# Kernel optimization log

Hardware: AMD Instinct MI355X
Metric: run time of the kernel (lower is better)

Reference implementation:

```python
import jax, jax.numpy as jnp
import numpy as np

TEMPERATURE = 0.5
SCALE_LOSS = 1.0 / 32.0
LAMBDA = 0.0039


def setup_inputs() -> dict:
    key = jax.random.key(0)
    z = jax.random.normal(key, (4096, 6, 256), dtype=jnp.float32)
    return {"z": z}


def reference(z):
    B, V = z.shape[0], z.shape[1]
    # [B, V, ...] -> [V, B, D], L2-normalize embeddings
    zv = z.reshape(B, V, -1).transpose(1, 0, 2)
    zn = zv / jnp.linalg.norm(zv, axis=-1, keepdims=True)

    # Positive error: per-sample cross-view similarity [B, V, V]
    sim_pos = jnp.einsum('vbd,wbd->bvw', zn, zn)
    pos = jnp.exp((1.0 - sim_pos) / TEMPERATURE).mean(axis=(1, 2))  # [B]

    # Negative error: per-view within-batch similarity [V, B, B]
    sim_neg = jnp.exp(jnp.einsum('vbd,vcd->vbc', zn, zn) / TEMPERATURE)
    offdiag_mask = ~jnp.eye(B, dtype=bool)  # [B, B]
    off_mean = jnp.where(offdiag_mask[None], sim_neg, 0.0).sum(-1) / (B - 1)  # [V, B]
    neg = off_mean.sum(0)  # [B], accumulated over views

    return jnp.sum(pos) * SCALE_LOSS + LAMBDA * jnp.sum(neg)
```

## Files before the change

### kernel.cpp

```cpp
#include <hip/hip_runtime.h>
#include <cstdint>
#include <cstddef>

#define B_N 4096
#define V_N 6
#define D_N 256
#define NTILE 528

typedef __bf16 bf16x8 __attribute__((ext_vector_type(8)));
typedef float f32x4 __attribute__((ext_vector_type(4)));

#define ALPHA 1.41421356237309515f

__device__ __forceinline__ unsigned short f2bf(float f) {
  unsigned int u = __float_as_uint(f);
  unsigned int r = (u + 0x7fffu + ((u >> 16) & 1u)) >> 16;
  return (unsigned short)r;
}

__device__ __forceinline__ void async_load16(void* lds, const void* gmem) {
  __builtin_amdgcn_global_load_lds(
      (const __attribute__((address_space(1))) unsigned int*)gmem,
      (__attribute__((address_space(3))) unsigned int*)lds,
      16, 0, 0);
}

__global__ __launch_bounds__(256) void norm_pos_kernel(
    const float* __restrict__ z, unsigned short* __restrict__ znb,
    float* __restrict__ pos_part) {
  const int b = blockIdx.x;
  const int t = threadIdx.x;
  const int lane = t & 63;
  const int w = t >> 6;

  __shared__ float zs[V_N][D_N];
  __shared__ float red[V_N][4];
  __shared__ float inv[V_N];
  __shared__ float pred[4];

  const float* zb = z + (size_t)b * (V_N * D_N);
#pragma unroll
  for (int v = 0; v < V_N; ++v) zs[v][t] = zb[v * D_N + t];
  __syncthreads();

#pragma unroll
  for (int v = 0; v < V_N; ++v) {
    float x = zs[v][t];
    float s = x * x;
#pragma unroll
    for (int off = 32; off > 0; off >>= 1) s += __shfl_down(s, off);
    if (lane == 0) red[v][w] = s;
  }
  __syncthreads();
  if (t < V_N) inv[t] = rsqrtf(red[t][0] + red[t][1] + red[t][2] + red[t][3]);
  __syncthreads();

#pragma unroll
  for (int v = 0; v < V_N; ++v) {
    float zn = zs[v][t] * inv[v] * ALPHA;
    znb[((size_t)v * B_N + b) * D_N + t] = f2bf(zn);
  }

  float psum = 0.0f;
  int pidx = 0;
#pragma unroll
  for (int v = 0; v < V_N; ++v) {
#pragma unroll
    for (int u = v + 1; u < V_N; ++u) {
      if ((pidx & 3) == w) {
        float s = 0.0f;
#pragma unroll
        for (int d = 0; d < D_N; d += 64) s += zs[v][lane + d] * zs[u][lane + d];
#pragma unroll
        for (int off = 32; off > 0; off >>= 1) s += __shfl_down(s, off);
        if (lane == 0) {
          float sim = s * inv[v] * inv[u];
          psum += __expf(2.0f * (1.0f - sim));
        }
      }
      ++pidx;
    }
  }
  if (lane == 0) pred[w] = psum;
  __syncthreads();
  if (t == 0) pos_part[b] = pred[0] + pred[1] + pred[2] + pred[3];
}

__global__ __launch_bounds__(256) void gram_kernel(
    const unsigned short* __restrict__ znb, float* __restrict__ neg_part) {
  const int v = blockIdx.y;
  const int t = blockIdx.x;
  int i = (int)((sqrtf(8.0f * (float)t + 1.0f) - 1.0f) * 0.5f);
  while ((i + 1) * (i + 2) / 2 <= t) ++i;
  while (i * (i + 1) / 2 > t) --i;
  const int j = t - i * (i + 1) / 2;

  const unsigned short* Zv = znb + (size_t)v * B_N * D_N;
  const unsigned short* Ag = Zv + (size_t)(i * 128) * D_N;
  const unsigned short* Bg = Zv + (size_t)(j * 128) * D_N;

  __shared__ __bf16 As[128][64];
  __shared__ __bf16 Bs[128][64];
  __shared__ float blk[4];

  const int tid = threadIdx.x;
  const int lane = tid & 63;
  const int w = tid >> 6;
  const int wr = w >> 1;
  const int wc = w & 1;

  const f32x4 vzero = {0.0f, 0.0f, 0.0f, 0.0f};
  f32x4 c[4][4];
#pragma unroll
  for (int a = 0; a < 4; ++a)
#pragma unroll
    for (int b2 = 0; b2 < 4; ++b2) c[a][b2] = vzero;

  const int kc = lane >> 4;
  const int mrow = wr * 64 + (lane & 15);
  const int ncol = wc * 64 + (lane & 15);

  __bf16* AsF = &As[0][0];
  __bf16* BsF = &Bs[0][0];

  for (int k0 = 0; k0 < D_N; k0 += 64) {
    __syncthreads();
#pragma unroll
    for (int q = 0; q < 4; ++q) {
      const int s = tid + 256 * q;
      const int row = s >> 3;
      const int gc = (s & 7) ^ (row & 7);
      async_load16(AsF + s * 8, Ag + (size_t)row * D_N + k0 + gc * 8);
      async_load16(BsF + s * 8, Bg + (size_t)row * D_N + k0 + gc * 8);
    }
    __syncthreads();

#pragma unroll
    for (int kk = 0; kk < 2; ++kk) {
      const int cbase = kk * 4 + kc;
      bf16x8 af[4], bfr[4];
#pragma unroll
      for (int f = 0; f < 4; ++f) {
        const int ra = mrow + 16 * f;
        const int rb2 = ncol + 16 * f;
        af[f]  = *(const bf16x8*)(AsF + ra * 64 + ((cbase ^ (ra & 7)) * 8));
        bfr[f] = *(const bf16x8*)(BsF + rb2 * 64 + ((cbase ^ (rb2 & 7)) * 8));
      }
#pragma unroll
      for (int fm = 0; fm < 4; ++fm)
#pragma unroll
        for (int fn = 0; fn < 4; ++fn)
          c[fm][fn] = __builtin_amdgcn_mfma_f32_16x16x32_bf16(
              af[fm], bfr[fn], c[fm][fn], 0, 0, 0);
    }
  }

  float lsum = 0.0f;
  const int rb = i * 128 + wr * 64 + (lane >> 4) * 4;
  const int cb = j * 128 + wc * 64 + (lane & 15);
#pragma unroll
  for (int fm = 0; fm < 4; ++fm) {
#pragma unroll
    for (int fn = 0; fn < 4; ++fn) {
      const int gcol = cb + fn * 16;
#pragma unroll
      for (int r = 0; r < 4; ++r) {
        const int grow = rb + fm * 16 + r;
        float e = __expf(c[fm][fn][r]);
        lsum += (grow == gcol) ? 0.0f : e;
      }
    }
  }
  if (i != j) lsum *= 2.0f;

#pragma unroll
  for (int off = 32; off > 0; off >>= 1) lsum += __shfl_down(lsum, off);
  if (lane == 0) blk[w] = lsum;
  __syncthreads();
  if (tid == 0) neg_part[t + NTILE * v] = blk[0] + blk[1] + blk[2] + blk[3];
}

__global__ __launch_bounds__(1024) void finalize_kernel(
    const float* __restrict__ pos_part, const float* __restrict__ neg_part,
    float* __restrict__ out) {
  const int t = threadIdx.x;
  const int lane = t & 63;
  const int w = t >> 6;
  __shared__ float pr[16], nr[16];

  float p = 0.0f;
  for (int idx = t; idx < B_N; idx += 1024) p += pos_part[idx];
  float n = 0.0f;
  for (int idx = t; idx < NTILE * V_N; idx += 1024) n += neg_part[idx];
#pragma unroll
  for (int off = 32; off > 0; off >>= 1) {
    p += __shfl_down(p, off);
    n += __shfl_down(n, off);
  }
  if (lane == 0) { pr[w] = p; nr[w] = n; }
  __syncthreads();
  if (t == 0) {
    float P = 0.0f, N = 0.0f;
#pragma unroll
    for (int k = 0; k < 16; ++k) { P += pr[k]; N += nr[k]; }
    out[0] = (1.0f / 32.0f) * ((float)B_N / 6.0f + P / 18.0f) +
             0.0039f * (N / (float)(B_N - 1));
  }
}

extern "C" void kernel_launch(void* const* d_in, const int* in_sizes, int n_in,
                              void* d_out, int out_size, void* d_ws, size_t ws_size,
                              hipStream_t stream) {
  const float* z = (const float*)d_in[0];
  float* out = (float*)d_out;
  float* pos_part = (float*)d_ws;
  float* neg_part = pos_part + B_N;
  unsigned short* znb = (unsigned short*)((char*)d_ws + 32768);

  norm_pos_kernel<<<B_N, 256, 0, stream>>>(z, znb, pos_part);
  dim3 grid(NTILE, V_N, 1);
  gram_kernel<<<grid, 256, 0, stream>>>(znb, neg_part);
  finalize_kernel<<<1, 1024, 0, stream>>>(pos_part, neg_part, out);
}
```

Measured before the change: 116.2 us.

## Quantize normalized embeddings to int8 and fuse finalize into gram kernel

Normalized embeddings are now quantized to int8 with a fixed scale instead of bf16, and the Gram matrix uses int8 MFMA (16x16x64), with the exponent argument rescaled by the inverse squared scale. This halves the memory traffic for the embeddings and doubles the MFMA throughput per instruction. The separate finalize kernel is replaced by a last-block reduction that uses an atomic counter reset by a memset, removing one launch but adding a memset. The int8 quantization adds precision error to the exponentiated similarities, which may affect accuracy tolerance.

```diff
diff --git a/kernel.cpp b/kernel.cpp
--- a/kernel.cpp
+++ b/kernel.cpp
@@ -6,17 +6,13 @@
 #define V_N 6
 #define D_N 256
 #define NTILE 528
-
-typedef __bf16 bf16x8 __attribute__((ext_vector_type(8)));
+#define NBLK (NTILE * V_N)
+
+typedef int i32x4 __attribute__((ext_vector_type(4)));
 typedef float f32x4 __attribute__((ext_vector_type(4)));
 
-#define ALPHA 1.41421356237309515f
-
-__device__ __forceinline__ unsigned short f2bf(float f) {
-  unsigned int u = __float_as_uint(f);
-  unsigned int r = (u + 0x7fffu + ((u >> 16) & 1u)) >> 16;
-  return (unsigned short)r;
-}
+#define QC 298.0f
+#define INV_C2_X2 (2.0f / (QC * QC))
 
 __device__ __forceinline__ void async_load16(void* lds, const void* gmem) {
   __builtin_amdgcn_global_load_lds(
@@ -26,7 +22,7 @@
 }
 
 __global__ __launch_bounds__(256) void norm_pos_kernel(
-    const float* __restrict__ z, unsigned short* __restrict__ znb,
+    const float* __restrict__ z, signed char* __restrict__ znb,
     float* __restrict__ pos_part) {
   const int b = blockIdx.x;
   const int t = threadIdx.x;
@@ -57,8 +53,9 @@
 
 #pragma unroll
   for (int v = 0; v < V_N; ++v) {
-    float zn = zs[v][t] * inv[v] * ALPHA;
-    znb[((size_t)v * B_N + b) * D_N + t] = f2bf(zn);
+    float q = rintf(zs[v][t] * inv[v] * QC);
+    q = fminf(127.0f, fmaxf(-127.0f, q));
+    znb[((size_t)v * B_N + b) * D_N + t] = (signed char)(int)q;
   }
 
   float psum = 0.0f;
@@ -87,7 +84,9 @@
 }
 
 __global__ __launch_bounds__(256) void gram_kernel(
-    const unsigned short* __restrict__ znb, float* __restrict__ neg_part) {
+    const signed char* __restrict__ znb, float* __restrict__ neg_part,
+    const float* __restrict__ pos_part, float* __restrict__ out,
+    int* __restrict__ counter) {
   const int v = blockIdx.y;
   const int t = blockIdx.x;
   int i = (int)((sqrtf(8.0f * (float)t + 1.0f) - 1.0f) * 0.5f);
@@ -95,13 +94,14 @@
   while (i * (i + 1) / 2 > t) --i;
   const int j = t - i * (i + 1) / 2;
 
-  const unsigned short* Zv = znb + (size_t)v * B_N * D_N;
-  const unsigned short* Ag = Zv + (size_t)(i * 128) * D_N;
-  const unsigned short* Bg = Zv + (size_t)(j * 128) * D_N;
-
-  __shared__ __bf16 As[128][64];
-  __shared__ __bf16 Bs[128][64];
-  __shared__ float blk[4];
+  const signed char* Zv = znb + (size_t)v * B_N * D_N;
+  const signed char* Ag = Zv + (size_t)(i * 128) * D_N;
+  const signed char* Bg = Zv + (size_t)(j * 128) * D_N;
+
+  __shared__ signed char As[128][128];
+  __shared__ signed char Bs[128][128];
+  __shared__ float blk[4], blk2[4];
+  __shared__ int is_last;
 
   const int tid = threadIdx.x;
   const int lane = tid & 63;
@@ -109,48 +109,47 @@
   const int wr = w >> 1;
   const int wc = w & 1;
 
-  const f32x4 vzero = {0.0f, 0.0f, 0.0f, 0.0f};
-  f32x4 c[4][4];
+  i32x4 c[4][4];
 #pragma unroll
   for (int a = 0; a < 4; ++a)
 #pragma unroll
-    for (int b2 = 0; b2 < 4; ++b2) c[a][b2] = vzero;
+    for (int b2 = 0; b2 < 4; ++b2) c[a][b2] = (i32x4){0, 0, 0, 0};
 
   const int kc = lane >> 4;
   const int mrow = wr * 64 + (lane & 15);
   const int ncol = wc * 64 + (lane & 15);
 
-  __bf16* AsF = &As[0][0];
-  __bf16* BsF = &Bs[0][0];
-
-  for (int k0 = 0; k0 < D_N; k0 += 64) {
+  signed char* AsF = &As[0][0];
+  signed char* BsF = &Bs[0][0];
+
+  for (int k0 = 0; k0 < D_N; k0 += 128) {
     __syncthreads();
 #pragma unroll
     for (int q = 0; q < 4; ++q) {
       const int s = tid + 256 * q;
       const int row = s >> 3;
       const int gc = (s & 7) ^ (row & 7);
-      async_load16(AsF + s * 8, Ag + (size_t)row * D_N + k0 + gc * 8);
-      async_load16(BsF + s * 8, Bg + (size_t)row * D_N + k0 + gc * 8);
+      async_load16(AsF + s * 16, Ag + (size_t)row * D_N + k0 + gc * 16);
+      async_load16(BsF + s * 16, Bg + (size_t)row * D_N + k0 + gc * 16);
     }
     __syncthreads();
 
 #pragma unroll
     for (int kk = 0; kk < 2; ++kk) {
       const int cbase = kk * 4 + kc;
-      bf16x8 af[4], bfr[4];
+      i32x4 af[4], bfr[4];
 #pragma unroll
       for (int f = 0; f < 4; ++f) {
         const int ra = mrow + 16 * f;
         const int rb2 = ncol + 16 * f;
-        af[f]  = *(const bf16x8*)(AsF + ra * 64 + ((cbase ^ (ra & 7)) * 8));
-        bfr[f] = *(const bf16x8*)(BsF + rb2 * 64 + ((cbase ^ (rb2 & 7)) * 8));
+        af[f]  = *(const i32x4*)(AsF + ra * 128 + ((cbase ^ (ra & 7)) * 16));
+        bfr[f] = *(const i32x4*)(BsF + rb2 * 128 + ((cbase ^ (rb2 & 7)) * 16));
       }
 #pragma unroll
       for (int fm = 0; fm < 4; ++fm)
 #pragma unroll
         for (int fn = 0; fn < 4; ++fn)
-          c[fm][fn] = __builtin_amdgcn_mfma_f32_16x16x32_bf16(
+          c[fm][fn] = __builtin_amdgcn_mfma_i32_16x16x64_i8(
               af[fm], bfr[fn], c[fm][fn], 0, 0, 0);
     }
   }
@@ -166,7 +165,7 @@
 #pragma unroll
       for (int r = 0; r < 4; ++r) {
         const int grow = rb + fm * 16 + r;
-        float e = __expf(c[fm][fn][r]);
+        float e = __expf((float)c[fm][fn][r] * INV_C2_X2);
         lsum += (grow == gcol) ? 0.0f : e;
       }
     }
@@ -177,34 +176,32 @@
   for (int off = 32; off > 0; off >>= 1) lsum += __shfl_down(lsum, off);
   if (lane == 0) blk[w] = lsum;
   __syncthreads();
-  if (tid == 0) neg_part[t + NTILE * v] = blk[0] + blk[1] + blk[2] + blk[3];
-}
-
-__global__ __launch_bounds__(1024) void finalize_kernel(
-    const float* __restrict__ pos_part, const float* __restrict__ neg_part,
-    float* __restrict__ out) {
-  const int t = threadIdx.x;
-  const int lane = t & 63;
-  const int w = t >> 6;
-  __shared__ float pr[16], nr[16];
-
-  float p = 0.0f;
-  for (int idx = t; idx < B_N; idx += 1024) p += pos_part[idx];
-  float n = 0.0f;
-  for (int idx = t; idx < NTILE * V_N; idx += 1024) n += neg_part[idx];
-#pragma unroll
-  for (int off = 32; off > 0; off >>= 1) {
-    p += __shfl_down(p, off);
-    n += __shfl_down(n, off);
-  }
-  if (lane == 0) { pr[w] = p; nr[w] = n; }
-  __syncthreads();
-  if (t == 0) {
-    float P = 0.0f, N = 0.0f;
-#pragma unroll
-    for (int k = 0; k < 16; ++k) { P += pr[k]; N += nr[k]; }
-    out[0] = (1.0f / 32.0f) * ((float)B_N / 6.0f + P / 18.0f) +
-             0.0039f * (N / (float)(B_N - 1));
+  if (tid == 0) {
+    neg_part[t + NTILE * v] = blk[0] + blk[1] + blk[2] + blk[3];
+    __threadfence();
+    is_last = (atomicAdd(counter, 1) == NBLK - 1);
+  }
+  __syncthreads();
+
+  if (is_last) {
+    __threadfence();
+    float p = 0.0f;
+    for (int idx = tid; idx < B_N; idx += 256) p += pos_part[idx];
+    float n = 0.0f;
+    for (int idx = tid; idx < NBLK; idx += 256) n += neg_part[idx];
+#pragma unroll
+    for (int off = 32; off > 0; off >>= 1) {
+      p += __shfl_down(p, off);
+      n += __shfl_down(n, off);
+    }
+    if (lane == 0) { blk[w] = p; blk2[w] = n; }
+    __syncthreads();
+    if (tid == 0) {
+      const float P = blk[0] + blk[1] + blk[2] + blk[3];
+      const float N = blk2[0] + blk2[1] + blk2[2] + blk2[3];
+      out[0] = (1.0f / 32.0f) * ((float)B_N / 6.0f + P / 18.0f) +
+               0.0039f * (N / (float)(B_N - 1));
+    }
   }
 }
 
@@ -213,12 +210,13 @@
                               hipStream_t stream) {
   const float* z = (const float*)d_in[0];
   float* out = (float*)d_out;
-  float* pos_part = (float*)d_ws;
+  int* counter = (int*)d_ws;
+  float* pos_part = (float*)((char*)d_ws + 256);
   float* neg_part = pos_part + B_N;
-  unsigned short* znb = (unsigned short*)((char*)d_ws + 32768);
-
+  signed char* znb = (signed char*)((char*)d_ws + 32768);
+
+  hipMemsetAsync(d_ws, 0, 256, stream);
   norm_pos_kernel<<<B_N, 256, 0, stream>>>(z, znb, pos_part);
   dim3 grid(NTILE, V_N, 1);
-  gram_kernel<<<grid, 256, 0, stream>>>(znb, neg_part);
-  finalize_kernel<<<1, 1024, 0, stream>>>(pos_part, neg_part, out);
-}
+  gram_kernel<<<grid, 256, 0, stream>>>(znb, neg_part, pos_part, out, counter);
+}
```

Measured after the change: 181.4 us. 56.0% more time.
